# Kernel optimization log

Hardware: AMD Instinct MI355X
Metric: run time of the kernel (lower is better)

## Reference

```python
import jax, jax.numpy as jnp
import numpy as np

DIM = 1024
HEADS = 16
HEAD_DIM = DIM // HEADS
SCALE = HEAD_DIM ** -0.5


def setup_inputs() -> dict:
    key = jax.random.key(0)
    k1, k2, k3, k4 = jax.random.split(key, 4)
    x = jax.random.normal(k1, (8, 1024, DIM), dtype=jnp.float32)
    # nn.Linear weight is [out, in]; init ~ small values
    W_qkv = jax.random.normal(k2, (3 * DIM, DIM), dtype=jnp.float32) * 0.02
    W_proj = jax.random.normal(k3, (DIM, DIM), dtype=jnp.float32) * 0.02
    b_proj = jax.random.normal(k4, (DIM,), dtype=jnp.float32) * 0.02
    return {"x": x, "W_qkv": W_qkv, "W_proj": W_proj, "b_proj": b_proj}


def reference(x, W_qkv, W_proj, b_proj):
    b, n, _ = x.shape
    h, d = HEADS, HEAD_DIM
    qkv = x @ W_qkv.T  # [b, n, 3*dim]
    # rearrange 'b n (qkv h d) -> qkv b h n d'
    qkv = qkv.reshape(b, n, 3, h, d).transpose(2, 0, 3, 1, 4)
    q, k, v = qkv[0], qkv[1], qkv[2]  # each [b, h, n, d]
    dots = jnp.einsum('bhid,bhjd->bhij', q, k) * SCALE
    attn = jax.nn.softmax(dots, axis=-1)
    out = jnp.einsum('bhij,bhjd->bhid', attn, v)
    out = out.transpose(0, 2, 1, 3).reshape(b, n, h * d)  # b n (h d)
    return out @ W_proj.T + b_proj
```

## Files before the change

kernel.cpp:

```cpp
#include <hip/hip_runtime.h>
#include <math.h>

#define DIM   1024
#define HEADS 16
#define HDIM  64
#define SEQ   1024
#define BATCH 8
#define QSCALE 0.1803368801111204f
#define LDH   72
#define ABM   128

typedef __attribute__((ext_vector_type(8))) short          short8_t;
typedef __attribute__((ext_vector_type(8))) unsigned short ushort8_t;
typedef __attribute__((ext_vector_type(4))) unsigned short ushort4_t;
typedef __attribute__((ext_vector_type(4))) float          floatx4;

__device__ __forceinline__ unsigned short f2bf(float f) {
    unsigned u = __float_as_uint(f);
    u += 0x7fffu + ((u >> 16) & 1u);
    return (unsigned short)(u >> 16);
}
__device__ __forceinline__ unsigned rnd_bf(float f) {
    unsigned u = __float_as_uint(f);
    return u + 0x7fffu + ((u >> 16) & 1u);
}
__device__ __forceinline__ float fast_exp2(float x) {
#if __has_builtin(__builtin_amdgcn_exp2f)
    return __builtin_amdgcn_exp2f(x);
#else
    return exp2f(x);
#endif
}
__device__ __forceinline__ void glds16(const unsigned short* g, unsigned short* l) {
    __builtin_amdgcn_global_load_lds(
        (const __attribute__((address_space(1))) void*)g,
        (__attribute__((address_space(3))) void*)l, 16, 0, 0);
}

__global__ __launch_bounds__(256) void cvt_bf16_all(const float* __restrict__ x,
                                                    const float* __restrict__ wqkv,
                                                    const float* __restrict__ wproj,
                                                    unsigned short* __restrict__ x_o,
                                                    unsigned short* __restrict__ wqkv_o,
                                                    unsigned short* __restrict__ wproj_o) {
    const int N8_X = BATCH * SEQ * DIM / 8;
    const int N8_WQ = 3 * DIM * DIM / 8;
    const int N8_WP = DIM * DIM / 8;
    int i = blockIdx.x * 256 + threadIdx.x;
    const float* in;
    unsigned short* out;
    if (i < N8_X)               { in = x;     out = x_o; }
    else if (i < N8_X + N8_WQ)  { i -= N8_X;  in = wqkv; out = wqkv_o; }
    else                        { i -= N8_X + N8_WQ;
                                  if (i >= N8_WP) return;
                                  in = wproj; out = wproj_o; }
    const float4* p = (const float4*)in + (size_t)i * 2;
    float4 a = p[0], b = p[1];
    ushort8_t u;
    u[0] = f2bf(a.x); u[1] = f2bf(a.y); u[2] = f2bf(a.z); u[3] = f2bf(a.w);
    u[4] = f2bf(b.x); u[5] = f2bf(b.y); u[6] = f2bf(b.z); u[7] = f2bf(b.w);
    ((ushort8_t*)out)[i] = u;
}

template<int MODE>
__global__ __launch_bounds__(256) void gemm_nt_mfma(const unsigned short* __restrict__ A,
                                                    const unsigned short* __restrict__ B,
                                                    const float* __restrict__ bias,
                                                    void* __restrict__ Cout,
                                                    unsigned short* __restrict__ vt,
                                                    int M, int N, int K) {
    __shared__ __align__(16) unsigned short As[128 * 32];
    __shared__ __align__(16) unsigned short Bs[128 * 32];

    const int tid  = threadIdx.x;
    const int lane = tid & 63;
    const int wave = tid >> 6;
    const int wm = (wave >> 1) * 64;
    const int wn = (wave & 1) * 64;
    const size_t brow = (size_t)blockIdx.y * 128;
    const size_t bcol = (size_t)blockIdx.x * 128;

    const int srow = lane >> 2;
    const int skc  = (lane & 3) * 8;
    const unsigned short* gA0 = A + (brow + wave * 16 + srow) * (size_t)K + skc;
    const unsigned short* gA1 = gA0 + (size_t)64 * K;
    const unsigned short* gB0 = B + (bcol + wave * 16 + srow) * (size_t)K + skc;
    const unsigned short* gB1 = gB0 + (size_t)64 * K;
    unsigned short* lA0 = &As[wave * 512 + lane * 8];
    unsigned short* lA1 = lA0 + 2048;
    unsigned short* lB0 = &Bs[wave * 512 + lane * 8];
    unsigned short* lB1 = lB0 + 2048;

    floatx4 acc[4][4];
    #pragma unroll
    for (int i = 0; i < 4; i++)
        #pragma unroll
        for (int j = 0; j < 4; j++) acc[i][j] = (floatx4){0.f, 0.f, 0.f, 0.f};

    const int kq = (lane >> 4) * 8;
    const int rr = lane & 15;

    for (int k0 = 0; k0 < K; k0 += 32) {
        __syncthreads();
        glds16(gA0 + k0, lA0);
        glds16(gA1 + k0, lA1);
        glds16(gB0 + k0, lB0);
        glds16(gB1 + k0, lB1);
        __syncthreads();

        short8_t af[4], bfr[4];
        #pragma unroll
        for (int mi = 0; mi < 4; mi++)
            af[mi] = *(const short8_t*)&As[(wm + mi * 16 + rr) * 32 + kq];
        #pragma unroll
        for (int ni = 0; ni < 4; ni++)
            bfr[ni] = *(const short8_t*)&Bs[(wn + ni * 16 + rr) * 32 + kq];

        #pragma unroll
        for (int mi = 0; mi < 4; mi++)
            #pragma unroll
            for (int ni = 0; ni < 4; ni++)
                acc[mi][ni] = __builtin_amdgcn_mfma_f32_16x16x32_bf16(
                    af[mi], bfr[ni], acc[mi][ni], 0, 0, 0);
    }

    const int crow = (lane >> 4) * 4;
    const int ccol = lane & 15;

    if (MODE == 0) {
        #pragma unroll
        for (int mi = 0; mi < 4; mi++)
            #pragma unroll
            for (int ni = 0; ni < 4; ni++) {
                const size_t col = bcol + wn + ni * 16 + ccol;
                const float bv = bias[col];
                #pragma unroll
                for (int r = 0; r < 4; r++) {
                    const size_t row = brow + wm + mi * 16 + crow + r;
                    ((float*)Cout)[row * N + col] = acc[mi][ni][r] + bv;
                }
            }
    } else {
        if (bcol < 2048) {
            const float sc = (bcol < 1024) ? QSCALE : 1.0f;
            unsigned short* qk = (unsigned short*)Cout;
            #pragma unroll
            for (int mi = 0; mi < 4; mi++)
                #pragma unroll
                for (int ni = 0; ni < 4; ni++) {
                    const size_t col = bcol + wn + ni * 16 + ccol;
                    #pragma unroll
                    for (int r = 0; r < 4; r++) {
                        const size_t row = brow + wm + mi * 16 + crow + r;
                        qk[row * 2048 + col] = f2bf(acc[mi][ni][r] * sc);
                    }
                }
        } else {
            #pragma unroll
            for (int mi = 0; mi < 4; mi++)
                #pragma unroll
                for (int ni = 0; ni < 4; ni++) {
                    const int dall = (int)(bcol + wn + ni * 16 + ccol) - 2048;
                    const int h = dall >> 6, d = dall & 63;
                    const size_t row0 = brow + wm + mi * 16 + crow;
                    const size_t bb = row0 >> 10;
                    const int n0 = (int)(row0 & 1023);
                    ushort4_t o;
                    #pragma unroll
                    for (int r = 0; r < 4; r++) o[r] = f2bf(acc[mi][ni][r]);
                    *(ushort4_t*)&vt[(((size_t)bb * HEADS + h) * HDIM + d) * SEQ + n0] = o;
                }
        }
    }
}

__global__ __launch_bounds__(256) void attn_mfma(const unsigned short* __restrict__ qk,
                                                 const unsigned short* __restrict__ vt,
                                                 unsigned short* __restrict__ aout) {
    const int qt = blockIdx.x;
    const int h  = blockIdx.y;
    const int b  = blockIdx.z;
    const int tid  = threadIdx.x;
    const int lane = tid & 63;
    const int wave = tid >> 6;
    const int g = lane >> 4;
    const int c = lane & 15;

    __shared__ __align__(16) unsigned short Qs[ABM * LDH];
    __shared__ __align__(16) unsigned short Ks[64 * LDH];
    __shared__ __align__(16) unsigned short Vs[64 * LDH];
    __shared__ float scr[4][2][16];

    {
        const int r  = tid >> 1;
        const int c0 = (tid & 1) * 32;
        const unsigned short* src =
            qk + ((size_t)(b * SEQ + qt * ABM + r)) * 2048 + h * HDIM + c0;
        unsigned short* dst = &Qs[r * LDH + c0];
        *(ushort8_t*)(dst)      = *(const ushort8_t*)(src);
        *(ushort8_t*)(dst + 8)  = *(const ushort8_t*)(src + 8);
        *(ushort8_t*)(dst + 16) = *(const ushort8_t*)(src + 16);
        *(ushort8_t*)(dst + 24) = *(const ushort8_t*)(src + 24);
    }
    __syncthreads();

    short8_t bq[2][2];
    #pragma unroll
    for (int f = 0; f < 2; f++)
        #pragma unroll
        for (int kc = 0; kc < 2; kc++)
            bq[f][kc] = *(const short8_t*)&Qs[(f * 64 + wave * 16 + c) * LDH + g * 8 + kc * 32];

    floatx4 O[2][4];
    #pragma unroll
    for (int f = 0; f < 2; f++)
        #pragma unroll
        for (int i = 0; i < 4; i++) O[f][i] = (floatx4){0.f, 0.f, 0.f, 0.f};
    float lsum[2] = {0.f, 0.f};

    const int sr = tid >> 2;
    const int sq = tid & 3;
    const unsigned short* ksrc0 =
        qk + ((size_t)(b * SEQ + sr)) * 2048 + DIM + h * HDIM + sq * 16;
    const unsigned short* vsrc0 =
        vt + (((size_t)(b * HEADS + h)) * HDIM + sr) * SEQ + sq * 16;

    for (int kt = 0; kt < SEQ / 64; kt++) {
        __syncthreads();
        {
            const unsigned short* ksrc = ksrc0 + (size_t)kt * 64 * 2048;
            const unsigned short* vsrc = vsrc0 + kt * 64;
            *(ushort8_t*)&Ks[sr * LDH + sq * 16]     = *(const ushort8_t*)ksrc;
            *(ushort8_t*)&Ks[sr * LDH + sq * 16 + 8] = *(const ushort8_t*)(ksrc + 8);
            *(ushort8_t*)&Vs[sr * LDH + sq * 16]     = *(const ushort8_t*)vsrc;
            *(ushort8_t*)&Vs[sr * LDH + sq * 16 + 8] = *(const ushort8_t*)(vsrc + 8);
        }
        __syncthreads();

        short8_t ak[4][2];
        #pragma unroll
        for (int nt = 0; nt < 4; nt++)
            #pragma unroll
            for (int kc = 0; kc < 2; kc++)
                ak[nt][kc] = *(const short8_t*)&Ks[(nt * 16 + c) * LDH + g * 8 + kc * 32];

        floatx4 S[2][4];
        #pragma unroll
        for (int f = 0; f < 2; f++)
            #pragma unroll
            for (int nt = 0; nt < 4; nt++) S[f][nt] = (floatx4){0.f, 0.f, 0.f, 0.f};
        #pragma unroll
        for (int f = 0; f < 2; f++)
            #pragma unroll
            for (int nt = 0; nt < 4; nt++)
                #pragma unroll
                for (int kc = 0; kc < 2; kc++)
                    S[f][nt] = __builtin_amdgcn_mfma_f32_16x16x32_bf16(
                        ak[nt][kc], bq[f][kc], S[f][nt], 0, 0, 0);

        #pragma unroll
        for (int f = 0; f < 2; f++)
            #pragma unroll
            for (int nt = 0; nt < 4; nt++) {
                const float p0 = fast_exp2(S[f][nt][0]);
                const float p1 = fast_exp2(S[f][nt][1]);
                const float p2 = fast_exp2(S[f][nt][2]);
                const float p3 = fast_exp2(S[f][nt][3]);
                lsum[f] += (p0 + p1) + (p2 + p3);
                const unsigned r01 = __builtin_amdgcn_perm(rnd_bf(p1), rnd_bf(p0), 0x07060302);
                const unsigned r23 = __builtin_amdgcn_perm(rnd_bf(p3), rnd_bf(p2), 0x07060302);
                *(uint2*)&Qs[(f * 64 + wave * 16 + c) * LDH + nt * 16 + g * 4] =
                    make_uint2(r01, r23);
            }

        short8_t bv[4][2];
        #pragma unroll
        for (int dnt = 0; dnt < 4; dnt++)
            #pragma unroll
            for (int kc = 0; kc < 2; kc++)
                bv[dnt][kc] = *(const short8_t*)&Vs[(dnt * 16 + c) * LDH + g * 8 + kc * 32];

        #pragma unroll
        for (int f = 0; f < 2; f++) {
            short8_t ap[2];
            #pragma unroll
            for (int kc = 0; kc < 2; kc++)
                ap[kc] = *(const short8_t*)&Qs[(f * 64 + wave * 16 + c) * LDH + g * 8 + kc * 32];
            #pragma unroll
            for (int dnt = 0; dnt < 4; dnt++)
                #pragma unroll
                for (int kc = 0; kc < 2; kc++)
                    O[f][dnt] = __builtin_amdgcn_mfma_f32_16x16x32_bf16(
                        ap[kc], bv[dnt][kc], O[f][dnt], 0, 0, 0);
        }
    }

    #pragma unroll
    for (int f = 0; f < 2; f++) {
        float s = lsum[f];
        s += __shfl_xor(s, 16);
        s += __shfl_xor(s, 32);
        if (g == 0) scr[wave][f][c] = 1.0f / s;
    }
    __builtin_amdgcn_s_waitcnt(0);

    #pragma unroll
    for (int f = 0; f < 2; f++) {
        const float4 inv4 = *(const float4*)&scr[wave][f][g * 4];
        #pragma unroll
        for (int r = 0; r < 4; r++) {
            const float invl = ((const float*)&inv4)[r];
            const size_t row = (size_t)b * SEQ + qt * ABM + f * 64 + wave * 16 + g * 4 + r;
            #pragma unroll
            for (int dnt = 0; dnt < 4; dnt++)
                aout[row * DIM + h * HDIM + dnt * 16 + c] = f2bf(O[f][dnt][r] * invl);
        }
    }
}

extern "C" void kernel_launch(void* const* d_in, const int* in_sizes, int n_in,
                              void* d_out, int out_size, void* d_ws, size_t ws_size,
                              hipStream_t stream) {
    const float* x      = (const float*)d_in[0];
    const float* W_qkv  = (const float*)d_in[1];
    const float* W_proj = (const float*)d_in[2];
    const float* b_proj = (const float*)d_in[3];
    float* out = (float*)d_out;

    const int M = BATCH * SEQ;

    unsigned short* ws       = (unsigned short*)d_ws;
    unsigned short* x_bf     = ws;
    unsigned short* wqkv_bf  = x_bf + (size_t)M * DIM;
    unsigned short* wproj_bf = wqkv_bf + (size_t)3 * DIM * DIM;
    unsigned short* qk_bf    = wproj_bf + (size_t)DIM * DIM;
    unsigned short* vt_bf    = qk_bf + (size_t)M * 2048;
    unsigned short* aout_bf  = vt_bf + (size_t)BATCH * HEADS * HDIM * SEQ;

    {
        const int n8 = (M * DIM + 3 * DIM * DIM + DIM * DIM) / 8;
        cvt_bf16_all<<<(n8 + 255) / 256, 256, 0, stream>>>(
            x, W_qkv, W_proj, x_bf, wqkv_bf, wproj_bf);
    }

    gemm_nt_mfma<2><<<dim3(3 * DIM / 128, M / 128), 256, 0, stream>>>(
        x_bf, wqkv_bf, nullptr, qk_bf, vt_bf, M, 3 * DIM, DIM);

    attn_mfma<<<dim3(SEQ / ABM, HEADS, BATCH), 256, 0, stream>>>(qk_bf, vt_bf, aout_bf);

    gemm_nt_mfma<0><<<dim3(DIM / 128, M / 128), 256, 0, stream>>>(
        aout_bf, wproj_bf, b_proj, out, nullptr, M, DIM, DIM);
}
```

Baseline: 275.3 us.

## Deepen GEMM K-tile with XOR-swizzled LDS and register-prefetch K/V in attention

The GEMM now loads a 64-wide K slice per iteration instead of 32, using an XOR swizzle on the 16-byte chunk index so the MFMA fragment reads from LDS avoid bank conflicts, which halves the barrier count. The attention kernel prefetches the next K/V tile into registers before the barrier and stores it to LDS on the following iteration, overlapping global loads with the MFMA work. The cost is doubled GEMM LDS use and more registers held live in attention, which may lower occupancy.

```diff
diff --git a/kernel.cpp b/kernel.cpp
--- a/kernel.cpp
+++ b/kernel.cpp
@@ -69,8 +69,8 @@
                                                     void* __restrict__ Cout,
                                                     unsigned short* __restrict__ vt,
                                                     int M, int N, int K) {
-    __shared__ __align__(16) unsigned short As[128 * 32];
-    __shared__ __align__(16) unsigned short Bs[128 * 32];
+    __shared__ __align__(16) unsigned short As[128 * 64];
+    __shared__ __align__(16) unsigned short Bs[128 * 64];
 
     const int tid  = threadIdx.x;
     const int lane = tid & 63;
@@ -80,16 +80,12 @@
     const size_t brow = (size_t)blockIdx.y * 128;
     const size_t bcol = (size_t)blockIdx.x * 128;
 
-    const int srow = lane >> 2;
-    const int skc  = (lane & 3) * 8;
-    const unsigned short* gA0 = A + (brow + wave * 16 + srow) * (size_t)K + skc;
-    const unsigned short* gA1 = gA0 + (size_t)64 * K;
-    const unsigned short* gB0 = B + (bcol + wave * 16 + srow) * (size_t)K + skc;
-    const unsigned short* gB1 = gB0 + (size_t)64 * K;
-    unsigned short* lA0 = &As[wave * 512 + lane * 8];
-    unsigned short* lA1 = lA0 + 2048;
-    unsigned short* lB0 = &Bs[wave * 512 + lane * 8];
-    unsigned short* lB1 = lB0 + 2048;
+    const int srow   = lane >> 3;
+    const int schunk = (lane & 7) ^ srow;
+    const unsigned short* gA = A + (brow + wave * 8 + srow) * (size_t)K + schunk * 8;
+    const unsigned short* gB = B + (bcol + wave * 8 + srow) * (size_t)K + schunk * 8;
+    unsigned short* lA = &As[wave * 512 + lane * 8];
+    unsigned short* lB = &Bs[wave * 512 + lane * 8];
 
     floatx4 acc[4][4];
     #pragma unroll
@@ -97,31 +93,36 @@
         #pragma unroll
         for (int j = 0; j < 4; j++) acc[i][j] = (floatx4){0.f, 0.f, 0.f, 0.f};
 
-    const int kq = (lane >> 4) * 8;
+    const int g  = lane >> 4;
     const int rr = lane & 15;
-
-    for (int k0 = 0; k0 < K; k0 += 32) {
+    const int xr = rr & 7;
+
+    for (int k0 = 0; k0 < K; k0 += 64) {
         __syncthreads();
-        glds16(gA0 + k0, lA0);
-        glds16(gA1 + k0, lA1);
-        glds16(gB0 + k0, lB0);
-        glds16(gB1 + k0, lB1);
+        #pragma unroll
+        for (int r = 0; r < 4; r++) {
+            glds16(gA + (size_t)r * 32 * K + k0, lA + r * 2048);
+            glds16(gB + (size_t)r * 32 * K + k0, lB + r * 2048);
+        }
         __syncthreads();
 
-        short8_t af[4], bfr[4];
-        #pragma unroll
-        for (int mi = 0; mi < 4; mi++)
-            af[mi] = *(const short8_t*)&As[(wm + mi * 16 + rr) * 32 + kq];
-        #pragma unroll
-        for (int ni = 0; ni < 4; ni++)
-            bfr[ni] = *(const short8_t*)&Bs[(wn + ni * 16 + rr) * 32 + kq];
-
-        #pragma unroll
-        for (int mi = 0; mi < 4; mi++)
+        #pragma unroll
+        for (int kc = 0; kc < 2; kc++) {
+            const int ch = ((kc * 4 + g) ^ xr) * 8;
+            short8_t af[4], bfr[4];
+            #pragma unroll
+            for (int mi = 0; mi < 4; mi++)
+                af[mi] = *(const short8_t*)&As[(wm + mi * 16 + rr) * 64 + ch];
             #pragma unroll
             for (int ni = 0; ni < 4; ni++)
-                acc[mi][ni] = __builtin_amdgcn_mfma_f32_16x16x32_bf16(
-                    af[mi], bfr[ni], acc[mi][ni], 0, 0, 0);
+                bfr[ni] = *(const short8_t*)&Bs[(wn + ni * 16 + rr) * 64 + ch];
+            #pragma unroll
+            for (int mi = 0; mi < 4; mi++)
+                #pragma unroll
+                for (int ni = 0; ni < 4; ni++)
+                    acc[mi][ni] = __builtin_amdgcn_mfma_f32_16x16x32_bf16(
+                        af[mi], bfr[ni], acc[mi][ni], 0, 0, 0);
+        }
     }
 
     const int crow = (lane >> 4) * 4;
@@ -191,6 +192,18 @@
     __shared__ __align__(16) unsigned short Vs[64 * LDH];
     __shared__ float scr[4][2][16];
 
+    const int sr = tid >> 2;
+    const int sq = tid & 3;
+    const unsigned short* ksrc0 =
+        qk + ((size_t)(b * SEQ + sr)) * 2048 + DIM + h * HDIM + sq * 16;
+    const unsigned short* vsrc0 =
+        vt + (((size_t)(b * HEADS + h)) * HDIM + sr) * SEQ + sq * 16;
+
+    ushort8_t ck0 = *(const ushort8_t*)ksrc0;
+    ushort8_t ck1 = *(const ushort8_t*)(ksrc0 + 8);
+    ushort8_t cv0 = *(const ushort8_t*)vsrc0;
+    ushort8_t cv1 = *(const ushort8_t*)(vsrc0 + 8);
+
     {
         const int r  = tid >> 1;
         const int c0 = (tid & 1) * 32;
@@ -218,23 +231,21 @@
         for (int i = 0; i < 4; i++) O[f][i] = (floatx4){0.f, 0.f, 0.f, 0.f};
     float lsum[2] = {0.f, 0.f};
 
-    const int sr = tid >> 2;
-    const int sq = tid & 3;
-    const unsigned short* ksrc0 =
-        qk + ((size_t)(b * SEQ + sr)) * 2048 + DIM + h * HDIM + sq * 16;
-    const unsigned short* vsrc0 =
-        vt + (((size_t)(b * HEADS + h)) * HDIM + sr) * SEQ + sq * 16;
-
     for (int kt = 0; kt < SEQ / 64; kt++) {
+        ushort8_t nk0, nk1, nv0, nv1;
+        if (kt + 1 < SEQ / 64) {
+            const unsigned short* ks = ksrc0 + (size_t)(kt + 1) * 64 * 2048;
+            const unsigned short* vs = vsrc0 + (kt + 1) * 64;
+            nk0 = *(const ushort8_t*)ks;
+            nk1 = *(const ushort8_t*)(ks + 8);
+            nv0 = *(const ushort8_t*)vs;
+            nv1 = *(const ushort8_t*)(vs + 8);
+        }
         __syncthreads();
-        {
-            const unsigned short* ksrc = ksrc0 + (size_t)kt * 64 * 2048;
-            const unsigned short* vsrc = vsrc0 + kt * 64;
-            *(ushort8_t*)&Ks[sr * LDH + sq * 16]     = *(const ushort8_t*)ksrc;
-            *(ushort8_t*)&Ks[sr * LDH + sq * 16 + 8] = *(const ushort8_t*)(ksrc + 8);
-            *(ushort8_t*)&Vs[sr * LDH + sq * 16]     = *(const ushort8_t*)vsrc;
-            *(ushort8_t*)&Vs[sr * LDH + sq * 16 + 8] = *(const ushort8_t*)(vsrc + 8);
-        }
+        *(ushort8_t*)&Ks[sr * LDH + sq * 16]     = ck0;
+        *(ushort8_t*)&Ks[sr * LDH + sq * 16 + 8] = ck1;
+        *(ushort8_t*)&Vs[sr * LDH + sq * 16]     = cv0;
+        *(ushort8_t*)&Vs[sr * LDH + sq * 16 + 8] = cv1;
         __syncthreads();
 
         short8_t ak[4][2];
@@ -293,6 +304,8 @@
                     O[f][dnt] = __builtin_amdgcn_mfma_f32_16x16x32_bf16(
                         ap[kc], bv[dnt][kc], O[f][dnt], 0, 0, 0);
         }
+
+        ck0 = nk0; ck1 = nk1; cv0 = nv0; cv1 = nv1;
     }
 
     #pragma unroll
```

Result: faster. 244.4 us (-11.2%).
